# Kernel optimization log

Hardware: AMD Instinct MI355X
Metric: run time of the kernel (lower is better)

## Reference

```python
import jax, jax.numpy as jnp
import numpy as np

HW = 16            # hardcoded hw_seq_len in the module
THETA = 10000.0

def _rope_tables(head_dim):
    # EVA VisionRotaryEmbeddingFast: per-axis rope dim = head_dim // 2
    hd = head_dim // 2
    inv_freq = 1.0 / (THETA ** (np.arange(0, hd, 2, dtype=np.float32) / hd))  # (hd//2,)
    t = np.arange(HW, dtype=np.float32)                # ft_seq_len == pt_seq_len
    f = np.einsum('i,j->ij', t, inv_freq)              # (HW, hd//2)
    f = np.repeat(f, 2, axis=-1)                       # (HW, hd)
    fx = np.broadcast_to(f[:, None, :], (HW, HW, hd))  # vary along rows
    fy = np.broadcast_to(f[None, :, :], (HW, HW, hd))  # vary along cols
    F = np.concatenate([fx, fy], axis=-1).reshape(HW * HW, head_dim)  # (256, head_dim)
    return jnp.asarray(np.cos(F)), jnp.asarray(np.sin(F))

def _rotate_half(x):
    # '... (d r) -> ... d r' with r=2; (x1, x2) -> (-x2, x1)
    x = x.reshape(*x.shape[:-1], -1, 2)
    x1, x2 = x[..., 0], x[..., 1]
    return jnp.stack((-x2, x1), axis=-1).reshape(*x.shape[:-2], -1)

def setup_inputs() -> dict:
    key = jax.random.key(0)
    k1, k2, k3 = jax.random.split(key, 3)
    B, N, C = 64, 256, 1024
    x = jax.random.normal(k1, (B, N, C), dtype=jnp.float32)
    qkv_w = jax.random.normal(k2, (3 * C, C), dtype=jnp.float32) * (C ** -0.5)
    proj_w = jax.random.normal(k3, (C, C), dtype=jnp.float32) * (C ** -0.5)
    proj_b = jnp.zeros((C,), dtype=jnp.float32)
    return {"x": x, "qkv_w": qkv_w, "proj_w": proj_w, "proj_b": proj_b}

def reference(x, qkv_w, proj_w, proj_b):
    B, N, C = x.shape
    H = 16
    D = C // H
    cos, sin = _rope_tables(D)  # (N, D) each; constants
    qkv = jnp.einsum('bnc,oc->bno', x, qkv_w).reshape(B, N, 3, H, D)
    qkv = jnp.transpose(qkv, (2, 0, 3, 1, 4))  # (3, B, H, N, D)
    q, k, v = qkv[0], qkv[1], qkv[2]
    q = q * cos + _rotate_half(q) * sin
    k = k * cos + _rotate_half(k) * sin
    scale = D ** -0.5
    scores = jnp.einsum('bhnd,bhmd->bhnm', q, k) * scale
    attn = jax.nn.softmax(scores, axis=-1)
    out = jnp.einsum('bhnm,bhmd->bhnd', attn, v)
    out = jnp.transpose(out, (0, 2, 1, 3)).reshape(B, N, C)
    return jnp.einsum('bnc,oc->bno', out, proj_w) + proj_b
```

## Files before the change

kernel.cpp:

```cpp
#include <hip/hip_runtime.h>
#include <stdint.h>

typedef __attribute__((ext_vector_type(8))) short bf16x8;
typedef __attribute__((ext_vector_type(4))) short bf16x4;
typedef __attribute__((ext_vector_type(4))) float f32x4;
typedef __attribute__((ext_vector_type(4))) unsigned short u16x4;

typedef __attribute__((address_space(3))) unsigned short lds_u16;
typedef const __attribute__((address_space(1))) unsigned short glb_u16;

__device__ __forceinline__ unsigned short f2bf(float f) {
  union { float f; unsigned u; } x; x.f = f;
  unsigned r = x.u + 0x7FFFu + ((x.u >> 16) & 1u);
  return (unsigned short)(r >> 16);
}

__global__ __launch_bounds__(256) void k_prep(const float* __restrict__ x,
                                              const float* __restrict__ wqkv,
                                              const float* __restrict__ wproj,
                                              unsigned short* __restrict__ xb,
                                              unsigned short* __restrict__ wqkvb,
                                              unsigned short* __restrict__ wprojb,
                                              float* __restrict__ cosT, float* __restrict__ sinT) {
  const int b = blockIdx.x;
  const float* in;
  unsigned short* out;
  int i;
  if (b < 16384) {
    in = x; out = xb; i = b * 256 + threadIdx.x;
  } else if (b < 16384 + 3072) {
    in = wqkv; out = wqkvb; i = (b - 16384) * 256 + threadIdx.x;
  } else if (b < 16384 + 3072 + 1024) {
    in = wproj; out = wprojb; i = (b - 16384 - 3072) * 256 + threadIdx.x;
  } else {
    int n = threadIdx.x;
    int r = n >> 4, cc = n & 15;
    for (int d = 0; d < 64; ++d) {
      int tpos = (d < 32) ? r : cc;
      int j = (d & 31) >> 1;
      float ang = (float)tpos * powf(10000.0f, -(float)j * (1.0f / 16.0f));
      cosT[n * 64 + d] = cosf(ang);
      sinT[n * 64 + d] = sinf(ang);
    }
    return;
  }
  f32x4 v = reinterpret_cast<const f32x4*>(in)[i];
  u16x4 o;
  o[0] = f2bf(v[0]); o[1] = f2bf(v[1]); o[2] = f2bf(v[2]); o[3] = f2bf(v[3]);
  reinterpret_cast<u16x4*>(out)[i] = o;
}

template <int EPI>
__global__ __launch_bounds__(512, 2) void k_gemm(
    const unsigned short* __restrict__ A,
    const unsigned short* __restrict__ B,
    int M, int N, int K, int nTM,
    const float* __restrict__ cosT, const float* __restrict__ sinT,
    unsigned short* __restrict__ qout, unsigned short* __restrict__ kout,
    unsigned short* __restrict__ vTout,
    const float* __restrict__ bias, float* __restrict__ fout) {
  __shared__ unsigned short smem_u16[65536];

  const int t = threadIdx.x, w = t >> 6, l = t & 63, c = l & 15, g = l >> 4;
  const int wm = w >> 2, wn = w & 3;

  const int nwg = gridDim.x;
  const int bid = (int)blockIdx.x;
  const int nTN = nwg / nTM;
  const int xcd = bid & 7;
  const int j = bid >> 3;
  const int tn = j % nTN;
  const int tm = xcd * (nTM >> 3) + j / nTN;
  const int m0 = tm * 256, n0 = tn * 256;

  const int rS = t >> 3;
  const int colS = (((t & 7) ^ ((t >> 3) & 7)) * 8);
  const unsigned short* Asrc = A + (size_t)(m0 + rS) * K + colS;
  const unsigned short* Bsrc = B + (size_t)(n0 + rS) * K + colS;
  const size_t hK = (size_t)128 * K;
  const size_t iK = (size_t)64 * K;

#define STG_A(db, half, i, kt)                                                              \
  __builtin_amdgcn_global_load_lds((glb_u16*)(Asrc + (half) * hK + (i) * iK + (kt) * 64),   \
      (lds_u16*)&smem_u16[((db) * 32768 + (half) * 16384 + (i) * 8192 + w * 1024) >> 1],    \
      16, 0, 0)
#define STG_B(db, half, i, kt)                                                                      \
  __builtin_amdgcn_global_load_lds((glb_u16*)(Bsrc + (half) * hK + (i) * iK + (kt) * 64),           \
      (lds_u16*)&smem_u16[(65536 + (db) * 32768 + (half) * 16384 + (i) * 8192 + w * 1024) >> 1],    \
      16, 0, 0)

#pragma unroll
  for (int kk = 0; kk < 2; ++kk) {
    STG_A(kk, 0, 0, kk); STG_A(kk, 0, 1, kk); STG_A(kk, 1, 0, kk); STG_A(kk, 1, 1, kk);
    STG_B(kk, 0, 0, kk); STG_B(kk, 0, 1, kk); STG_B(kk, 1, 0, kk); STG_B(kk, 1, 1, kk);
  }

  f32x4 acc[8][4];
#pragma unroll
  for (int i = 0; i < 8; ++i)
#pragma unroll
    for (int jj = 0; jj < 4; ++jj) acc[i][jj] = 0.0f;

  const int xm7 = (c & 7) << 4;
  const int ko0 = (g * 16) ^ xm7;
  const int ko1 = (g * 16 + 64) ^ xm7;
  const int rAb = (wm * 128 + c) * 128;
  const int rBb = (wn * 64 + c) * 128;

  bf16x8 a0[4][2], a1[4][2], bq[4][2];

#define RD_A0(Abo)                                                                       \
  _Pragma("unroll") for (int mf = 0; mf < 4; ++mf) {                                     \
    a0[mf][0] = *(const bf16x8*)&smem_u16[((Abo) + rAb + mf * 2048 + ko0) >> 1];         \
    a0[mf][1] = *(const bf16x8*)&smem_u16[((Abo) + rAb + mf * 2048 + ko1) >> 1];         \
  }
#define RD_A1(Abo)                                                                       \
  _Pragma("unroll") for (int mf = 0; mf < 4; ++mf) {                                     \
    a1[mf][0] = *(const bf16x8*)&smem_u16[((Abo) + rAb + (mf + 4) * 2048 + ko0) >> 1];   \
    a1[mf][1] = *(const bf16x8*)&smem_u16[((Abo) + rAb + (mf + 4) * 2048 + ko1) >> 1];   \
  }
#define RD_BLO(Bbo)                                                                      \
  _Pragma("unroll") for (int nf = 0; nf < 2; ++nf) {                                     \
    bq[nf][0] = *(const bf16x8*)&smem_u16[((Bbo) + rBb + nf * 2048 + ko0) >> 1];         \
    bq[nf][1] = *(const bf16x8*)&smem_u16[((Bbo) + rBb + nf * 2048 + ko1) >> 1];         \
  }
#define RD_BHI(Bbo)                                                                      \
  _Pragma("unroll") for (int nf = 2; nf < 4; ++nf) {                                     \
    bq[nf][0] = *(const bf16x8*)&smem_u16[((Bbo) + rBb + nf * 2048 + ko0) >> 1];         \
    bq[nf][1] = *(const bf16x8*)&smem_u16[((Bbo) + rBb + nf * 2048 + ko1) >> 1];         \
  }
#define MFMA_Q(am, bl, bh, mo)                                                           \
  __builtin_amdgcn_s_setprio(1);                                                         \
  _Pragma("unroll") for (int mf = 0; mf < 4; ++mf)                                       \
  _Pragma("unroll") for (int nf = (bl); nf < (bh); ++nf)                                 \
  _Pragma("unroll") for (int ks = 0; ks < 2; ++ks)                                       \
      acc[mf + (mo)][nf] =                                                               \
          __builtin_amdgcn_mfma_f32_16x16x32_bf16(am[mf][ks], bq[nf][ks], acc[mf + (mo)][nf], 0, 0, 0); \
  __builtin_amdgcn_s_setprio(0)

  asm volatile("s_waitcnt vmcnt(8)" ::: "memory");
  __builtin_amdgcn_s_barrier();
  asm volatile("" ::: "memory");
  RD_A0(0);
  RD_BLO(65536);

  const int nKT = K >> 6;
  for (int k = 0; k < nKT; ++k) {
    const int db = k & 1;
    const int Abo = db * 32768;
    const int Bbo = 65536 + db * 32768;
    const int nAbo = (db ^ 1) * 32768;
    const int nBbo = 65536 + (db ^ 1) * 32768;
    const int k2 = k + 2;
    const bool st = (k2 < nKT);

    asm volatile("s_waitcnt lgkmcnt(0)" ::: "memory");
    RD_BHI(Bbo);
    MFMA_Q(a0, 0, 2, 0);
    __builtin_amdgcn_s_barrier();
    asm volatile("" ::: "memory");

    RD_A1(Abo);
    asm volatile("s_waitcnt lgkmcnt(8)" ::: "memory");
    if (st) { STG_A(db, 0, 0, k2); STG_A(db, 1, 0, k2); }
    MFMA_Q(a0, 2, 4, 0);
    __builtin_amdgcn_s_barrier();
    asm volatile("" ::: "memory");

    asm volatile("s_waitcnt lgkmcnt(0)" ::: "memory");
    if (st) { STG_B(db, 0, 0, k2); STG_B(db, 0, 1, k2); STG_B(db, 1, 0, k2); STG_B(db, 1, 1, k2); }
    MFMA_Q(a1, 0, 2, 4);
    __builtin_amdgcn_s_barrier();
    asm volatile("" ::: "memory");

    if (st) { STG_A(db, 0, 1, k2); STG_A(db, 1, 1, k2); }
    if (k < nKT - 2) {
      asm volatile("s_waitcnt vmcnt(8)" ::: "memory");
    } else if (k == nKT - 2) {
      asm volatile("s_waitcnt vmcnt(0)" ::: "memory");
    }
    __builtin_amdgcn_s_barrier();
    asm volatile("" ::: "memory");
    if (k + 1 < nKT) { RD_A0(nAbo); RD_BLO(nBbo); }
    __builtin_amdgcn_sched_barrier(0);
    MFMA_Q(a1, 2, 4, 4);
    __builtin_amdgcn_s_barrier();
    asm volatile("" ::: "memory");
  }
#undef STG_A
#undef STG_B
#undef RD_A0
#undef RD_A1
#undef RD_BLO
#undef RD_BHI
#undef MFMA_Q

  if constexpr (EPI == 0) {
    const int which = n0 >> 10;
    unsigned short* qk = (which == 0) ? qout : kout;
#pragma unroll
    for (int nf = 0; nf < 4; ++nf) {
      const int o = n0 + wn * 64 + nf * 16 + c;
      const int h = (o >> 6) & 15;
      const int d = o & 63;
      if (which < 2) {
        const float sgn = (d & 1) ? 1.0f : -1.0f;
        const float qscale = (which == 0) ? 0.125f : 1.0f;
#pragma unroll
        for (int mf = 0; mf < 8; ++mf) {
          const int m = m0 + wm * 128 + mf * 16 + g * 4;
          const int bb = m >> 8;
          const int nb = m & 255;
          f32x4 v = acc[mf][nf];
          f32x4 p;
          p[0] = __shfl_xor(v[0], 1);
          p[1] = __shfl_xor(v[1], 1);
          p[2] = __shfl_xor(v[2], 1);
          p[3] = __shfl_xor(v[3], 1);
          size_t base = ((size_t)(bb * 16 + h) * 256 + nb) * 64 + d;
#pragma unroll
          for (int jj = 0; jj < 4; ++jj) {
            const int n = nb + jj;
            const float cv = cosT[n * 64 + d];
            const float sv = sinT[n * 64 + d];
            float ov = (v[jj] * cv + sgn * p[jj] * sv) * qscale;
            qk[base + (size_t)jj * 64] = f2bf(ov);
          }
        }
      } else {
#pragma unroll
        for (int mf = 0; mf < 8; ++mf) {
          const int m = m0 + wm * 128 + mf * 16 + g * 4;
          const int bb = m >> 8;
          const int nb = m & 255;
          f32x4 v = acc[mf][nf];
          u16x4 pk;
          pk[0] = f2bf(v[0]); pk[1] = f2bf(v[1]); pk[2] = f2bf(v[2]); pk[3] = f2bf(v[3]);
          size_t idx = ((size_t)(bb * 16 + h) * 64 + d) * 256 + nb;
          *reinterpret_cast<u16x4*>(vTout + idx) = pk;
        }
      }
    }
  } else {
#pragma unroll
    for (int nf = 0; nf < 4; ++nf) {
      const int o = n0 + wn * 64 + nf * 16 + c;
      const float bv = bias[o];
#pragma unroll
      for (int mf = 0; mf < 8; ++mf) {
        const int m = m0 + wm * 128 + mf * 16 + g * 4;
        f32x4 v = acc[mf][nf];
#pragma unroll
        for (int jj = 0; jj < 4; ++jj) fout[(size_t)(m + jj) * N + o] = v[jj] + bv;
      }
    }
  }
}

__global__ __launch_bounds__(256) void k_attn(const unsigned short* __restrict__ Q,
                                              const unsigned short* __restrict__ Kb,
                                              const unsigned short* __restrict__ VT,
                                              unsigned short* __restrict__ Out) {
  constexpr int LDK = 80, LDP = 80;
  __shared__ unsigned short klds[64 * LDK];
  __shared__ unsigned short plds[4][64 * LDP];
  const int bh = blockIdx.x;
  const int bb = bh >> 4, h = bh & 15;
  const int t = threadIdx.x, w = t >> 6, l = t & 63, c = l & 15, g = l >> 4;
  const unsigned short* qh = Q + (size_t)bh * 256 * 64;
  const unsigned short* kh = Kb + (size_t)bh * 256 * 64;
  const unsigned short* vh = VT + (size_t)bh * 64 * 256;
  const int q0 = w * 64;

  bf16x8 qf[4][2];
#pragma unroll
  for (int nf = 0; nf < 4; ++nf)
#pragma unroll
    for (int ks = 0; ks < 2; ++ks)
      qf[nf][ks] = *reinterpret_cast<const bf16x8*>(qh + (q0 + nf * 16 + c) * 64 + ks * 32 + g * 8);

  f32x4 oacc[4][4];
#pragma unroll
  for (int i = 0; i < 4; ++i)
#pragma unroll
    for (int jj = 0; jj < 4; ++jj) oacc[i][jj] = 0.0f;
  float mr[4] = {-1e30f, -1e30f, -1e30f, -1e30f};
  float lr[4] = {0.f, 0.f, 0.f, 0.f};

  for (int ch = 0; ch < 4; ++ch) {
    __syncthreads();
    {
      int row = t >> 3, col = (t & 7) * 8;
#pragma unroll
      for (int rep = 0; rep < 2; ++rep) {
        int r = rep * 32 + row;
        bf16x8 kv = *reinterpret_cast<const bf16x8*>(kh + (ch * 64 + r) * 64 + col);
        *reinterpret_cast<bf16x8*>(&klds[r * LDK + col]) = kv;
      }
    }
    __syncthreads();

    f32x4 s[4][4];
#pragma unroll
    for (int i = 0; i < 4; ++i)
#pragma unroll
      for (int jj = 0; jj < 4; ++jj) s[i][jj] = 0.0f;
#pragma unroll
    for (int ks = 0; ks < 2; ++ks) {
      bf16x8 kf[4];
#pragma unroll
      for (int mf = 0; mf < 4; ++mf)
        kf[mf] = *reinterpret_cast<const bf16x8*>(&klds[(mf * 16 + c) * LDK + ks * 32 + g * 8]);
#pragma unroll
      for (int mf = 0; mf < 4; ++mf)
#pragma unroll
        for (int nf = 0; nf < 4; ++nf)
          s[mf][nf] = __builtin_amdgcn_mfma_f32_16x16x32_bf16(kf[mf], qf[nf][ks], s[mf][nf], 0, 0, 0);
    }

#pragma unroll
    for (int nf = 0; nf < 4; ++nf) {
      float mx = -1e30f;
#pragma unroll
      for (int mf = 0; mf < 4; ++mf)
#pragma unroll
        for (int jj = 0; jj < 4; ++jj) mx = fmaxf(mx, s[mf][nf][jj]);
      mx = fmaxf(mx, __shfl_xor(mx, 16));
      mx = fmaxf(mx, __shfl_xor(mx, 32));
      float mnew = fmaxf(mr[nf], mx);
      float rsc = __expf(mr[nf] - mnew);
      mr[nf] = mnew;
      float sum = 0.f;
#pragma unroll
      for (int mf = 0; mf < 4; ++mf)
#pragma unroll
        for (int jj = 0; jj < 4; ++jj) {
          float p = __expf(s[mf][nf][jj] - mnew);
          s[mf][nf][jj] = p;
          sum += p;
        }
      sum += __shfl_xor(sum, 16);
      sum += __shfl_xor(sum, 32);
      lr[nf] = lr[nf] * rsc + sum;
#pragma unroll
      for (int mf = 0; mf < 4; ++mf) oacc[mf][nf] *= rsc;
    }

#pragma unroll
    for (int mf = 0; mf < 4; ++mf)
#pragma unroll
      for (int nf = 0; nf < 4; ++nf) {
        bf16x4 pk;
        pk[0] = (short)f2bf(s[mf][nf][0]);
        pk[1] = (short)f2bf(s[mf][nf][1]);
        pk[2] = (short)f2bf(s[mf][nf][2]);
        pk[3] = (short)f2bf(s[mf][nf][3]);
        *reinterpret_cast<bf16x4*>(&plds[w][(nf * 16 + c) * LDP + mf * 16 + g * 4]) = pk;
      }

#pragma unroll
    for (int ks = 0; ks < 2; ++ks) {
      bf16x8 vf[4], pf[4];
#pragma unroll
      for (int mf = 0; mf < 4; ++mf)
        vf[mf] = *reinterpret_cast<const bf16x8*>(vh + (mf * 16 + c) * 256 + ch * 64 + ks * 32 + g * 8);
#pragma unroll
      for (int nf = 0; nf < 4; ++nf) {
        bf16x4 p0 = *reinterpret_cast<const bf16x4*>(&plds[w][(nf * 16 + c) * LDP + ks * 32 + g * 8]);
        bf16x4 p1 = *reinterpret_cast<const bf16x4*>(&plds[w][(nf * 16 + c) * LDP + ks * 32 + g * 8 + 4]);
        pf[nf] = __builtin_shufflevector(p0, p1, 0, 1, 2, 3, 4, 5, 6, 7);
      }
#pragma unroll
      for (int mf = 0; mf < 4; ++mf)
#pragma unroll
        for (int nf = 0; nf < 4; ++nf)
          oacc[mf][nf] = __builtin_amdgcn_mfma_f32_16x16x32_bf16(vf[mf], pf[nf], oacc[mf][nf], 0, 0, 0);
    }
  }

  float linv[4];
#pragma unroll
  for (int nf = 0; nf < 4; ++nf) linv[nf] = 1.0f / lr[nf];
#pragma unroll
  for (int mf = 0; mf < 4; ++mf)
#pragma unroll
    for (int nf = 0; nf < 4; ++nf) {
      f32x4 v = oacc[mf][nf];
      u16x4 pk;
      pk[0] = f2bf(v[0] * linv[nf]);
      pk[1] = f2bf(v[1] * linv[nf]);
      pk[2] = f2bf(v[2] * linv[nf]);
      pk[3] = f2bf(v[3] * linv[nf]);
      size_t row = (size_t)bb * 256 + q0 + nf * 16 + c;
      size_t idx = row * 1024 + (size_t)h * 64 + mf * 16 + g * 4;
      *reinterpret_cast<u16x4*>(Out + idx) = pk;
    }
}

extern "C" void kernel_launch(void* const* d_in, const int* in_sizes, int n_in,
                              void* d_out, int out_size, void* d_ws, size_t ws_size,
                              hipStream_t stream) {
  const float* x = (const float*)d_in[0];
  const float* wqkv = (const float*)d_in[1];
  const float* wproj = (const float*)d_in[2];
  const float* bproj = (const float*)d_in[3];

  char* ws = (char*)d_ws;
  unsigned short* xb = (unsigned short*)(ws);
  unsigned short* wqkvb = (unsigned short*)(ws + 33554432);
  unsigned short* wprojb = (unsigned short*)(ws + 39845888);
  float* cosT = (float*)(ws + 41943040);
  float* sinT = (float*)(ws + 42008576);
  unsigned short* qb = (unsigned short*)(ws + 42074112);
  unsigned short* kb = (unsigned short*)(ws + 75628544);
  unsigned short* vtb = (unsigned short*)(ws + 109182976);
  unsigned short* attn_out = xb;

  k_prep<<<16384 + 3072 + 1024 + 1, 256, 0, stream>>>(x, wqkv, wproj, xb, wqkvb, wprojb,
                                                      cosT, sinT);

  k_gemm<0><<<64 * 12, 512, 0, stream>>>(xb, wqkvb, 16384, 3072, 1024, 64,
                                         cosT, sinT, qb, kb, vtb, nullptr, nullptr);
  k_attn<<<1024, 256, 0, stream>>>(qb, kb, vtb, attn_out);
  k_gemm<1><<<64 * 4, 512, 0, stream>>>(attn_out, wprojb, 16384, 1024, 1024, 64,
                                        nullptr, nullptr, nullptr, nullptr, nullptr,
                                        bproj, (float*)d_out);
}
```

Measured before the change: 275.2 us.

## Shrink GEMM tiles to 128x128 with simpler double-buffered loop and higher occupancy

Changes both GEMM kernels from 256x256 output tiles to 128x128 tiles. LDS drops to 64KB and launch bounds allow 4 blocks per CU. The four-phase interleaved LDS-read/MFMA schedule is replaced by a plain load-all-fragments-then-compute loop. The aim is more workgroups and better CU occupancy, which matters most for the proj GEMM that launched only 256 blocks. The cost is lower arithmetic intensity per tile, more global and LDS traffic, and less overlap of LDS reads with MFMA.

```diff
diff --git a/kernel.cpp b/kernel.cpp
--- a/kernel.cpp
+++ b/kernel.cpp
@@ -51,7 +51,7 @@
 }
 
 template <int EPI>
-__global__ __launch_bounds__(512, 2) void k_gemm(
+__global__ __launch_bounds__(512, 4) void k_gemm(
     const unsigned short* __restrict__ A,
     const unsigned short* __restrict__ B,
     int M, int N, int K, int nTM,
@@ -59,7 +59,7 @@
     unsigned short* __restrict__ qout, unsigned short* __restrict__ kout,
     unsigned short* __restrict__ vTout,
     const float* __restrict__ bias, float* __restrict__ fout) {
-  __shared__ unsigned short smem_u16[65536];
+  __shared__ unsigned short smem_u16[32768];
 
   const int t = threadIdx.x, w = t >> 6, l = t & 63, c = l & 15, g = l >> 4;
   const int wm = w >> 2, wn = w & 3;
@@ -71,144 +71,102 @@
   const int j = bid >> 3;
   const int tn = j % nTN;
   const int tm = xcd * (nTM >> 3) + j / nTN;
-  const int m0 = tm * 256, n0 = tn * 256;
+  const int m0 = tm * 128, n0 = tn * 128;
 
   const int rS = t >> 3;
-  const int colS = (((t & 7) ^ ((t >> 3) & 7)) * 8);
+  const int colS = ((t & 7) ^ ((t >> 3) & 7)) * 8;
   const unsigned short* Asrc = A + (size_t)(m0 + rS) * K + colS;
   const unsigned short* Bsrc = B + (size_t)(n0 + rS) * K + colS;
-  const size_t hK = (size_t)128 * K;
   const size_t iK = (size_t)64 * K;
 
-#define STG_A(db, half, i, kt)                                                              \
-  __builtin_amdgcn_global_load_lds((glb_u16*)(Asrc + (half) * hK + (i) * iK + (kt) * 64),   \
-      (lds_u16*)&smem_u16[((db) * 32768 + (half) * 16384 + (i) * 8192 + w * 1024) >> 1],    \
-      16, 0, 0)
-#define STG_B(db, half, i, kt)                                                                      \
-  __builtin_amdgcn_global_load_lds((glb_u16*)(Bsrc + (half) * hK + (i) * iK + (kt) * 64),           \
-      (lds_u16*)&smem_u16[(65536 + (db) * 32768 + (half) * 16384 + (i) * 8192 + w * 1024) >> 1],    \
-      16, 0, 0)
+#define STG_A(db, i, kt)                                                              \
+  __builtin_amdgcn_global_load_lds((glb_u16*)(Asrc + (i) * iK + (kt) * 64),           \
+      (lds_u16*)&smem_u16[((db) * 16384 + (i) * 8192 + w * 1024) >> 1], 16, 0, 0)
+#define STG_B(db, i, kt)                                                              \
+  __builtin_amdgcn_global_load_lds((glb_u16*)(Bsrc + (i) * iK + (kt) * 64),           \
+      (lds_u16*)&smem_u16[(32768 + (db) * 16384 + (i) * 8192 + w * 1024) >> 1], 16, 0, 0)
 
 #pragma unroll
   for (int kk = 0; kk < 2; ++kk) {
-    STG_A(kk, 0, 0, kk); STG_A(kk, 0, 1, kk); STG_A(kk, 1, 0, kk); STG_A(kk, 1, 1, kk);
-    STG_B(kk, 0, 0, kk); STG_B(kk, 0, 1, kk); STG_B(kk, 1, 0, kk); STG_B(kk, 1, 1, kk);
-  }
-
-  f32x4 acc[8][4];
-#pragma unroll
-  for (int i = 0; i < 8; ++i)
-#pragma unroll
-    for (int jj = 0; jj < 4; ++jj) acc[i][jj] = 0.0f;
+    STG_A(kk, 0, kk); STG_A(kk, 1, kk);
+    STG_B(kk, 0, kk); STG_B(kk, 1, kk);
+  }
+
+  f32x4 acc[4][2];
+#pragma unroll
+  for (int i = 0; i < 4; ++i)
+#pragma unroll
+    for (int jj = 0; jj < 2; ++jj) acc[i][jj] = 0.0f;
 
   const int xm7 = (c & 7) << 4;
   const int ko0 = (g * 16) ^ xm7;
   const int ko1 = (g * 16 + 64) ^ xm7;
-  const int rAb = (wm * 128 + c) * 128;
-  const int rBb = (wn * 64 + c) * 128;
-
-  bf16x8 a0[4][2], a1[4][2], bq[4][2];
-
-#define RD_A0(Abo)                                                                       \
-  _Pragma("unroll") for (int mf = 0; mf < 4; ++mf) {                                     \
-    a0[mf][0] = *(const bf16x8*)&smem_u16[((Abo) + rAb + mf * 2048 + ko0) >> 1];         \
-    a0[mf][1] = *(const bf16x8*)&smem_u16[((Abo) + rAb + mf * 2048 + ko1) >> 1];         \
-  }
-#define RD_A1(Abo)                                                                       \
-  _Pragma("unroll") for (int mf = 0; mf < 4; ++mf) {                                     \
-    a1[mf][0] = *(const bf16x8*)&smem_u16[((Abo) + rAb + (mf + 4) * 2048 + ko0) >> 1];   \
-    a1[mf][1] = *(const bf16x8*)&smem_u16[((Abo) + rAb + (mf + 4) * 2048 + ko1) >> 1];   \
-  }
-#define RD_BLO(Bbo)                                                                      \
-  _Pragma("unroll") for (int nf = 0; nf < 2; ++nf) {                                     \
-    bq[nf][0] = *(const bf16x8*)&smem_u16[((Bbo) + rBb + nf * 2048 + ko0) >> 1];         \
-    bq[nf][1] = *(const bf16x8*)&smem_u16[((Bbo) + rBb + nf * 2048 + ko1) >> 1];         \
-  }
-#define RD_BHI(Bbo)                                                                      \
-  _Pragma("unroll") for (int nf = 2; nf < 4; ++nf) {                                     \
-    bq[nf][0] = *(const bf16x8*)&smem_u16[((Bbo) + rBb + nf * 2048 + ko0) >> 1];         \
-    bq[nf][1] = *(const bf16x8*)&smem_u16[((Bbo) + rBb + nf * 2048 + ko1) >> 1];         \
-  }
-#define MFMA_Q(am, bl, bh, mo)                                                           \
-  __builtin_amdgcn_s_setprio(1);                                                         \
-  _Pragma("unroll") for (int mf = 0; mf < 4; ++mf)                                       \
-  _Pragma("unroll") for (int nf = (bl); nf < (bh); ++nf)                                 \
-  _Pragma("unroll") for (int ks = 0; ks < 2; ++ks)                                       \
-      acc[mf + (mo)][nf] =                                                               \
-          __builtin_amdgcn_mfma_f32_16x16x32_bf16(am[mf][ks], bq[nf][ks], acc[mf + (mo)][nf], 0, 0, 0); \
-  __builtin_amdgcn_s_setprio(0)
-
-  asm volatile("s_waitcnt vmcnt(8)" ::: "memory");
+  const int rAb = (wm * 64 + c) * 128;
+  const int rBb = (wn * 32 + c) * 128;
+
+  asm volatile("s_waitcnt vmcnt(4)" ::: "memory");
   __builtin_amdgcn_s_barrier();
   asm volatile("" ::: "memory");
-  RD_A0(0);
-  RD_BLO(65536);
-
+
+  bf16x8 af[4][2], bfq[2][2];
   const int nKT = K >> 6;
   for (int k = 0; k < nKT; ++k) {
     const int db = k & 1;
-    const int Abo = db * 32768;
-    const int Bbo = 65536 + db * 32768;
-    const int nAbo = (db ^ 1) * 32768;
-    const int nBbo = 65536 + (db ^ 1) * 32768;
+    const int Abo = db * 16384;
+    const int Bbo = 32768 + db * 16384;
     const int k2 = k + 2;
     const bool st = (k2 < nKT);
 
+#pragma unroll
+    for (int mf = 0; mf < 4; ++mf) {
+      af[mf][0] = *(const bf16x8*)&smem_u16[(Abo + rAb + mf * 2048 + ko0) >> 1];
+      af[mf][1] = *(const bf16x8*)&smem_u16[(Abo + rAb + mf * 2048 + ko1) >> 1];
+    }
+#pragma unroll
+    for (int nf = 0; nf < 2; ++nf) {
+      bfq[nf][0] = *(const bf16x8*)&smem_u16[(Bbo + rBb + nf * 2048 + ko0) >> 1];
+      bfq[nf][1] = *(const bf16x8*)&smem_u16[(Bbo + rBb + nf * 2048 + ko1) >> 1];
+    }
     asm volatile("s_waitcnt lgkmcnt(0)" ::: "memory");
-    RD_BHI(Bbo);
-    MFMA_Q(a0, 0, 2, 0);
     __builtin_amdgcn_s_barrier();
     asm volatile("" ::: "memory");
 
-    RD_A1(Abo);
-    asm volatile("s_waitcnt lgkmcnt(8)" ::: "memory");
-    if (st) { STG_A(db, 0, 0, k2); STG_A(db, 1, 0, k2); }
-    MFMA_Q(a0, 2, 4, 0);
+    if (st) { STG_A(db, 0, k2); STG_A(db, 1, k2); STG_B(db, 0, k2); STG_B(db, 1, k2); }
+    __builtin_amdgcn_s_setprio(1);
+#pragma unroll
+    for (int mf = 0; mf < 4; ++mf)
+#pragma unroll
+      for (int nf = 0; nf < 2; ++nf)
+#pragma unroll
+        for (int ks = 0; ks < 2; ++ks)
+          acc[mf][nf] = __builtin_amdgcn_mfma_f32_16x16x32_bf16(af[mf][ks], bfq[nf][ks], acc[mf][nf], 0, 0, 0);
+    __builtin_amdgcn_s_setprio(0);
+
+    if (k < nKT - 2) {
+      asm volatile("s_waitcnt vmcnt(4)" ::: "memory");
+    } else if (k == nKT - 2) {
+      asm volatile("s_waitcnt vmcnt(0)" ::: "memory");
+    }
     __builtin_amdgcn_s_barrier();
     asm volatile("" ::: "memory");
-
-    asm volatile("s_waitcnt lgkmcnt(0)" ::: "memory");
-    if (st) { STG_B(db, 0, 0, k2); STG_B(db, 0, 1, k2); STG_B(db, 1, 0, k2); STG_B(db, 1, 1, k2); }
-    MFMA_Q(a1, 0, 2, 4);
-    __builtin_amdgcn_s_barrier();
-    asm volatile("" ::: "memory");
-
-    if (st) { STG_A(db, 0, 1, k2); STG_A(db, 1, 1, k2); }
-    if (k < nKT - 2) {
-      asm volatile("s_waitcnt vmcnt(8)" ::: "memory");
-    } else if (k == nKT - 2) {
-      asm volatile("s_waitcnt vmcnt(0)" ::: "memory");
-    }
-    __builtin_amdgcn_s_barrier();
-    asm volatile("" ::: "memory");
-    if (k + 1 < nKT) { RD_A0(nAbo); RD_BLO(nBbo); }
-    __builtin_amdgcn_sched_barrier(0);
-    MFMA_Q(a1, 2, 4, 4);
-    __builtin_amdgcn_s_barrier();
-    asm volatile("" ::: "memory");
   }
 #undef STG_A
 #undef STG_B
-#undef RD_A0
-#undef RD_A1
-#undef RD_BLO
-#undef RD_BHI
-#undef MFMA_Q
 
   if constexpr (EPI == 0) {
     const int which = n0 >> 10;
     unsigned short* qk = (which == 0) ? qout : kout;
 #pragma unroll
-    for (int nf = 0; nf < 4; ++nf) {
-      const int o = n0 + wn * 64 + nf * 16 + c;
+    for (int nf = 0; nf < 2; ++nf) {
+      const int o = n0 + wn * 32 + nf * 16 + c;
       const int h = (o >> 6) & 15;
       const int d = o & 63;
       if (which < 2) {
         const float sgn = (d & 1) ? 1.0f : -1.0f;
         const float qscale = (which == 0) ? 0.125f : 1.0f;
 #pragma unroll
-        for (int mf = 0; mf < 8; ++mf) {
-          const int m = m0 + wm * 128 + mf * 16 + g * 4;
+        for (int mf = 0; mf < 4; ++mf) {
+          const int m = m0 + wm * 64 + mf * 16 + g * 4;
           const int bb = m >> 8;
           const int nb = m & 255;
           f32x4 v = acc[mf][nf];
@@ -229,8 +187,8 @@
         }
       } else {
 #pragma unroll
-        for (int mf = 0; mf < 8; ++mf) {
-          const int m = m0 + wm * 128 + mf * 16 + g * 4;
+        for (int mf = 0; mf < 4; ++mf) {
+          const int m = m0 + wm * 64 + mf * 16 + g * 4;
           const int bb = m >> 8;
           const int nb = m & 255;
           f32x4 v = acc[mf][nf];
@@ -243,12 +201,12 @@
     }
   } else {
 #pragma unroll
-    for (int nf = 0; nf < 4; ++nf) {
-      const int o = n0 + wn * 64 + nf * 16 + c;
+    for (int nf = 0; nf < 2; ++nf) {
+      const int o = n0 + wn * 32 + nf * 16 + c;
       const float bv = bias[o];
 #pragma unroll
-      for (int mf = 0; mf < 8; ++mf) {
-        const int m = m0 + wm * 128 + mf * 16 + g * 4;
+      for (int mf = 0; mf < 4; ++mf) {
+        const int m = m0 + wm * 64 + mf * 16 + g * 4;
         f32x4 v = acc[mf][nf];
 #pragma unroll
         for (int jj = 0; jj < 4; ++jj) fout[(size_t)(m + jj) * N + o] = v[jj] + bv;
@@ -419,10 +377,10 @@
   k_prep<<<16384 + 3072 + 1024 + 1, 256, 0, stream>>>(x, wqkv, wproj, xb, wqkvb, wprojb,
                                                       cosT, sinT);
 
-  k_gemm<0><<<64 * 12, 512, 0, stream>>>(xb, wqkvb, 16384, 3072, 1024, 64,
-                                         cosT, sinT, qb, kb, vtb, nullptr, nullptr);
+  k_gemm<0><<<128 * 24, 512, 0, stream>>>(xb, wqkvb, 16384, 3072, 1024, 128,
+                                          cosT, sinT, qb, kb, vtb, nullptr, nullptr);
   k_attn<<<1024, 256, 0, stream>>>(qb, kb, vtb, attn_out);
-  k_gemm<1><<<64 * 4, 512, 0, stream>>>(attn_out, wprojb, 16384, 1024, 1024, 64,
-                                        nullptr, nullptr, nullptr, nullptr, nullptr,
-                                        bproj, (float*)d_out);
-}
+  k_gemm<1><<<128 * 8, 512, 0, stream>>>(attn_out, wprojb, 16384, 1024, 1024, 128,
+                                         nullptr, nullptr, nullptr, nullptr, nullptr,
+                                         bproj, (float*)d_out);
+}
```

Result: slower. 298.2 us (+8.3%).
